# Kernel optimization log

Measured on AMD Instinct MI355X. Metric: run time of the kernel, lower is better.

The kernel has to match this reference:

```python
import jax, jax.numpy as jnp
import numpy as np

LN_EPS = 1e-5  # torch nn.LayerNorm default

def _layer_norm(x, g, b):
    mu = x.mean(axis=-1, keepdims=True)
    var = x.var(axis=-1, keepdims=True)
    return (x - mu) / jnp.sqrt(var + LN_EPS) * g + b

def setup_inputs() -> dict:
    key = jax.random.key(0)
    ks = jax.random.split(key, 8)
    B, T, L = 1, 4, 384
    c_z, c_t, H, C = 128, 64, 4, 16
    s = 0.02
    t = jax.random.normal(ks[0], (B, T, L, L, c_t), dtype=jnp.float32)
    z = jax.random.normal(ks[1], (B, L, L, c_z), dtype=jnp.float32)
    template_mask = jax.random.randint(ks[2], (B, T, L), 0, 2).astype(jnp.float32)
    Wq = jax.random.normal(ks[3], (c_z, H * C), dtype=jnp.float32) * s
    Wk = jax.random.normal(ks[4], (c_t, H * C), dtype=jnp.float32) * s
    Wv = jax.random.normal(ks[5], (c_t, H * C), dtype=jnp.float32) * s
    Wo = jax.random.normal(ks[6], (H * C, c_z), dtype=jnp.float32) * s
    bo = jnp.zeros((c_z,), dtype=jnp.float32)
    z_ln_g = jnp.ones((c_z,), dtype=jnp.float32)
    z_ln_b = jnp.zeros((c_z,), dtype=jnp.float32)
    t_ln_g = jnp.ones((c_t,), dtype=jnp.float32)
    t_ln_b = jnp.zeros((c_t,), dtype=jnp.float32)
    return dict(t=t, z=z, template_mask=template_mask,
                z_ln_g=z_ln_g, z_ln_b=z_ln_b, t_ln_g=t_ln_g, t_ln_b=t_ln_b,
                Wq=Wq, Wk=Wk, Wv=Wv, Wo=Wo, bo=bo)

def reference(t, z, template_mask, z_ln_g, z_ln_b, t_ln_g, t_ln_b, Wq, Wk, Wv, Wo, bo):
    B, T, L = t.shape[0], t.shape[1], t.shape[2]
    H, C = 4, 16
    z_norm = _layer_norm(z, z_ln_g, z_ln_b)          # [B,L,L,c_z]
    t_norm = _layer_norm(t, t_ln_g, t_ln_b)          # [B,T,L,L,c_t]
    q = (z_norm @ Wq).reshape(B, L, L, H, C)          # [B,L,L,H,C]
    k = (t_norm @ Wk).reshape(B, T, L, L, H, C)       # [B,T,L,L,H,C]
    v = (t_norm @ Wv).reshape(B, T, L, L, H, C)
    logits = jnp.einsum('bijhc,btijhc->btijh', q, k) / jnp.sqrt(jnp.float32(C))
    # pair_mask[b,t,i,j] = m[b,t,i]*m[b,t,j]
    pair_mask = template_mask[:, :, :, None] * template_mask[:, :, None, :]  # [B,T,L,L]
    logits = jnp.where(pair_mask[..., None] == 0, jnp.float32(-1e9), logits)
    attn = jax.nn.softmax(logits, axis=1)             # softmax over template dim T
    attn = attn * pair_mask[..., None]
    attn = attn / jnp.clip(attn.sum(axis=1, keepdims=True), 1e-8, None)
    out = jnp.einsum('btijh,btijhc->bijhc', attn, v).reshape(B, L, L, H * C)
    return out @ Wo + bo
```

## Files before the change

### kernel.cpp

```cpp
#include <hip/hip_runtime.h>

typedef unsigned int u32;
typedef unsigned short u16;
typedef __attribute__((ext_vector_type(8))) short short8;
typedef __attribute__((ext_vector_type(4))) float f4;

#define MFMA(a, b, c) __builtin_amdgcn_mfma_f32_16x16x32_bf16((a), (b), (c), 0, 0, 0)
#define LL 384
#define NPAIR 147456

__device__ __forceinline__ u16 f2bf(float f) {
    u32 u = __float_as_uint(f);
    u = (u + 0x7fffu + ((u >> 16) & 1u)) >> 16;
    return (u16)u;
}
__device__ __forceinline__ u32 pack2(float a, float b) {
    u32 ua = __float_as_uint(a); ua = (ua + 0x7fffu + ((ua >> 16) & 1u)) >> 16;
    u32 ub = __float_as_uint(b); ub = (ub + 0x7fffu + ((ub >> 16) & 1u)) >> 16;
    return ua | (ub << 16);
}
__device__ __forceinline__ short8 ld8(const u16* p) { return *reinterpret_cast<const short8*>(p); }

template <int CTRL>
__device__ __forceinline__ float dpp_add(float v) {
    int t = __builtin_amdgcn_update_dpp(0, __float_as_int(v), CTRL, 0xf, 0xf, true);
    return v + __int_as_float(t);
}
__device__ __forceinline__ float red16(float v) {
    v = dpp_add<0xB1>(v);
    v = dpp_add<0x4E>(v);
    v = dpp_add<0x124>(v);
    v = dpp_add<0x128>(v);
    return v;
}


__global__ void prep_w(const float* __restrict__ Wq, const float* __restrict__ Wk,
                       const float* __restrict__ Wv, const float* __restrict__ Wo,
                       const float* __restrict__ zg, const float* __restrict__ tg,
                       float* __restrict__ ws) {
    int idx = blockIdx.x * blockDim.x + threadIdx.x;
    u16* wsu = (u16*)ws;
    if (idx < 8192) {
        int kb = idx >> 9, rem = idx & 511, n = rem >> 3, j = rem & 7, k = kb * 8 + j;
        wsu[idx] = f2bf(Wq[k * 64 + n] * zg[k]);
    } else if (idx < 12288) {
        int e = idx - 8192;
        int kb = e >> 9, rem = e & 511, n = rem >> 3, j = rem & 7, k = kb * 8 + j;
        wsu[idx] = f2bf(Wk[k * 64 + n] * tg[k]);
    } else if (idx < 16384) {
        int e = idx - 12288;
        int kb = e >> 9, rem = e & 511, n = rem >> 3, j = rem & 7, k = kb * 8 + j;
        wsu[idx] = f2bf(Wv[k * 64 + n] * tg[k]);
    } else if (idx < 24576) {
        int e = idx - 16384;
        int kb = e >> 10, rem = e & 1023, n = rem >> 3, j = rem & 7, k = kb * 8 + j;
        wsu[idx] = f2bf(Wo[k * 128 + n]);
    }
}

__global__ void prep_aux(const float* __restrict__ Wq, const float* __restrict__ Wk,
                         const float* __restrict__ Wv, const float* __restrict__ zg,
                         const float* __restrict__ zb, const float* __restrict__ tg,
                         const float* __restrict__ tb, const float* __restrict__ bo,
                         float* __restrict__ ws) {
    int idx = blockIdx.x * blockDim.x + threadIdx.x;
    if (idx < 384) {
        int g = idx >> 6, hc = idx & 63;
        float acc = 0.f;
        if (g == 0)      { for (int d = 0; d < 128; ++d) acc += zg[d] * Wq[d*64+hc]; ws[12288+hc] = acc; }
        else if (g == 1) { for (int d = 0; d < 128; ++d) acc += zb[d] * Wq[d*64+hc]; ws[12352+hc] = acc; }
        else if (g == 2) { for (int d = 0; d < 64;  ++d) acc += tg[d] * Wk[d*64+hc]; ws[12416+hc] = acc; }
        else if (g == 3) { for (int d = 0; d < 64;  ++d) acc += tb[d] * Wk[d*64+hc]; ws[12480+hc] = acc; }
        else if (g == 4) { for (int d = 0; d < 64;  ++d) acc += tg[d] * Wv[d*64+hc]; ws[12544+hc] = acc; }
        else             { for (int d = 0; d < 64;  ++d) acc += tb[d] * Wv[d*64+hc]; ws[12608+hc] = acc; }
    } else if (idx < 512) {
        ws[12672 + idx - 384] = bo[idx - 384];
    }
}

__global__ __launch_bounds__(256, 5) void tpa_main(
    const float* __restrict__ tmpl,
    const float* __restrict__ z,
    const float* __restrict__ mask,
    const float* __restrict__ ws,
    float* __restrict__ out)
{
    __shared__ __align__(16) u16 sT[4 * 32 * 72];
    __shared__ __align__(16) u16 sZ[32 * 136];
    __shared__ float sZr[32], sZrm[32];
    __shared__ float sTr[4 * 32], sTrm[4 * 32];
    __shared__ float sAux[384];
    __shared__ float sBo[128];
    __shared__ float sPm[4 * 32];

    const int tid = threadIdx.x;
    const int p0 = blockIdx.x * 32;
    const u16* wsu = (const u16*)ws;

    if (tid < 128) {
        sAux[tid]       = ws[12288 + tid];
        sAux[128 + tid] = ws[12416 + tid];
        sAux[256 + tid] = ws[12544 + tid];
        sBo[tid]        = ws[12672 + tid];
        int tt = tid >> 5, rr = tid & 31;
        int p = p0 + rr, i = p / LL, j = p - i * LL;
        sPm[tt * 32 + rr] = mask[tt * LL + i] * mask[tt * LL + j];
    }
    {
        int pp = tid >> 3, part = tid & 7;
        const float4* zg4 = (const float4*)(z + (size_t)(p0 + pp) * 128) + part * 4;
        float4 a0 = zg4[0], a1 = zg4[1], a2 = zg4[2], a3 = zg4[3];
        float s = a0.x+a0.y+a0.z+a0.w + a1.x+a1.y+a1.z+a1.w
                + a2.x+a2.y+a2.z+a2.w + a3.x+a3.y+a3.z+a3.w;
        float ss = a0.x*a0.x+a0.y*a0.y+a0.z*a0.z+a0.w*a0.w
                 + a1.x*a1.x+a1.y*a1.y+a1.z*a1.z+a1.w*a1.w
                 + a2.x*a2.x+a2.y*a2.y+a2.z*a2.z+a2.w*a2.w
                 + a3.x*a3.x+a3.y*a3.y+a3.z*a3.z+a3.w*a3.w;
        s += __shfl_xor(s, 1); ss += __shfl_xor(ss, 1);
        s += __shfl_xor(s, 2); ss += __shfl_xor(ss, 2);
        s += __shfl_xor(s, 4); ss += __shfl_xor(ss, 4);
        if (part == 0) {
            float mu = s * (1.f / 128.f);
            float var = fmaf(-mu, mu, ss * (1.f / 128.f));
            float r = rsqrtf(var + 1e-5f);
            sZr[pp] = r; sZrm[pp] = r * mu;
        }
        uint4 w0, w1;
        w0.x = pack2(a0.x, a0.y); w0.y = pack2(a0.z, a0.w);
        w0.z = pack2(a1.x, a1.y); w0.w = pack2(a1.z, a1.w);
        w1.x = pack2(a2.x, a2.y); w1.y = pack2(a2.z, a2.w);
        w1.z = pack2(a3.x, a3.y); w1.w = pack2(a3.z, a3.w);
        uint4* d = (uint4*)(sZ + pp * 136 + part * 16);
        d[0] = w0; d[1] = w1;
    }
    {
        int tt = tid >> 6, pp = (tid >> 1) & 31, part = tid & 1;
        const float4* tg4 = (const float4*)(tmpl + ((size_t)tt * NPAIR + p0 + pp) * 64) + part * 8;
        float s = 0.f, ss = 0.f;
        uint4 wbuf[4];
        #pragma unroll
        for (int c = 0; c < 4; ++c) {
            float4 b0 = tg4[c * 2], b1 = tg4[c * 2 + 1];
            s  += b0.x+b0.y+b0.z+b0.w + b1.x+b1.y+b1.z+b1.w;
            ss += b0.x*b0.x+b0.y*b0.y+b0.z*b0.z+b0.w*b0.w
                + b1.x*b1.x+b1.y*b1.y+b1.z*b1.z+b1.w*b1.w;
            wbuf[c].x = pack2(b0.x, b0.y); wbuf[c].y = pack2(b0.z, b0.w);
            wbuf[c].z = pack2(b1.x, b1.y); wbuf[c].w = pack2(b1.z, b1.w);
        }
        s += __shfl_xor(s, 1); ss += __shfl_xor(ss, 1);
        if (part == 0) {
            float mu = s * (1.f / 64.f);
            float var = fmaf(-mu, mu, ss * (1.f / 64.f));
            float r = rsqrtf(var + 1e-5f);
            sTr[tt * 32 + pp] = r; sTrm[tt * 32 + pp] = r * mu;
        }
        uint4* d = (uint4*)(sT + tt * 2304 + pp * 72 + part * 32);
        d[0] = wbuf[0]; d[1] = wbuf[1]; d[2] = wbuf[2]; d[3] = wbuf[3];
    }
    __syncthreads();

    const int wave = tid >> 6, lane = tid & 63, g = lane >> 4, l15 = lane & 15;
    const int rt = wave & 1, nh = wave >> 1;
    const int rowA = rt * 16 + l15;
    const int col0 = (2 * nh) * 16 + l15, col1 = (2 * nh + 1) * 16 + l15;
    int rowC[4];
    #pragma unroll
    for (int r = 0; r < 4; ++r) rowC[r] = rt * 16 + g * 4 + r;

    f4 aq0 = {0.f,0.f,0.f,0.f}, aq1 = {0.f,0.f,0.f,0.f};
    #pragma unroll
    for (int ks = 0; ks < 4; ++ks) {
        short8 A = ld8(sZ + rowA * 136 + ks * 32 + g * 8);
        const u16* wb = wsu + (ks * 4 + g) * 512;
        aq0 = MFMA(A, ld8(wb + col0 * 8), aq0);
        aq1 = MFMA(A, ld8(wb + col1 * 8), aq1);
    }
    float qv[2][4];
    {
        float GQ0 = sAux[col0], BQ0 = sAux[64 + col0];
        float GQ1 = sAux[col1], BQ1 = sAux[64 + col1];
        #pragma unroll
        for (int r = 0; r < 4; ++r) {
            float zr = sZr[rowC[r]], zm = sZrm[rowC[r]];
            qv[0][r] = 0.25f * fmaf(zr, aq0[r], fmaf(-zm, GQ0, BQ0));
            qv[1][r] = 0.25f * fmaf(zr, aq1[r], fmaf(-zm, GQ1, BQ1));
        }
    }

    float lg[4][2][4];
    {
        const u16* wk = wsu + 8192;
        short8 Bk00 = ld8(wk + g * 512 + col0 * 8);
        short8 Bk01 = ld8(wk + g * 512 + col1 * 8);
        short8 Bk10 = ld8(wk + (4 + g) * 512 + col0 * 8);
        short8 Bk11 = ld8(wk + (4 + g) * 512 + col1 * 8);
        float GK0 = sAux[128 + col0], BK0 = sAux[192 + col0];
        float GK1 = sAux[128 + col1], BK1 = sAux[192 + col1];
        #pragma unroll
        for (int tt = 0; tt < 4; ++tt) {
            const u16* At = sT + tt * 2304 + rowA * 72;
            short8 A0 = ld8(At + g * 8);
            short8 A1 = ld8(At + 32 + g * 8);
            f4 k0 = {0.f,0.f,0.f,0.f}, k1 = {0.f,0.f,0.f,0.f};
            k0 = MFMA(A0, Bk00, k0); k1 = MFMA(A0, Bk01, k1);
            k0 = MFMA(A1, Bk10, k0); k1 = MFMA(A1, Bk11, k1);
            #pragma unroll
            for (int r = 0; r < 4; ++r) {
                float tr = sTr[tt * 32 + rowC[r]], tm = sTrm[tt * 32 + rowC[r]];
                float kc0 = fmaf(tr, k0[r], fmaf(-tm, GK0, BK0));
                float kc1 = fmaf(tr, k1[r], fmaf(-tm, GK1, BK1));
                lg[tt][0][r] = red16(qv[0][r] * kc0);
                lg[tt][1][r] = red16(qv[1][r] * kc1);
            }
        }
    }

    float ap[4][2][4], cb[2][4], cg[2][4];
    #pragma unroll
    for (int r = 0; r < 4; ++r) {
        float trA[4], tmA[4], pmA[4];
        #pragma unroll
        for (int tt = 0; tt < 4; ++tt) {
            trA[tt] = sTr[tt * 32 + rowC[r]];
            tmA[tt] = sTrm[tt * 32 + rowC[r]];
            pmA[tt] = sPm[tt * 32 + rowC[r]];
        }
        #pragma unroll
        for (int nn = 0; nn < 2; ++nn) {
            float l0 = lg[0][nn][r], l1 = lg[1][nn][r], l2 = lg[2][nn][r], l3 = lg[3][nn][r];
            float mx = fmaxf(fmaxf(l0, l1), fmaxf(l2, l3));
            float e0 = __expf(l0 - mx) * pmA[0];
            float e1 = __expf(l1 - mx) * pmA[1];
            float e2 = __expf(l2 - mx) * pmA[2];
            float e3 = __expf(l3 - mx) * pmA[3];
            float s = (e0 + e1) + (e2 + e3);
            float rr = __builtin_amdgcn_rcpf(fmaxf(s, 1e-20f));
            float a0 = e0 * rr, a1 = e1 * rr, a2 = e2 * rr, a3 = e3 * rr;
            cb[nn][r] = s * rr;
            cg[nn][r] = a0 * tmA[0] + a1 * tmA[1] + a2 * tmA[2] + a3 * tmA[3];
            ap[0][nn][r] = a0 * trA[0]; ap[1][nn][r] = a1 * trA[1];
            ap[2][nn][r] = a2 * trA[2]; ap[3][nn][r] = a3 * trA[3];
        }
    }

    float o0[4] = {0.f,0.f,0.f,0.f}, o1[4] = {0.f,0.f,0.f,0.f};
    {
        const u16* wv = wsu + 12288;
        short8 Bv00 = ld8(wv + g * 512 + col0 * 8);
        short8 Bv01 = ld8(wv + g * 512 + col1 * 8);
        short8 Bv10 = ld8(wv + (4 + g) * 512 + col0 * 8);
        short8 Bv11 = ld8(wv + (4 + g) * 512 + col1 * 8);
        #pragma unroll
        for (int tt = 0; tt < 4; ++tt) {
            const u16* At = sT + tt * 2304 + rowA * 72;
            short8 A0 = ld8(At + g * 8);
            short8 A1 = ld8(At + 32 + g * 8);
            f4 v0 = {0.f,0.f,0.f,0.f}, v1 = {0.f,0.f,0.f,0.f};
            v0 = MFMA(A0, Bv00, v0); v1 = MFMA(A0, Bv01, v1);
            v0 = MFMA(A1, Bv10, v0); v1 = MFMA(A1, Bv11, v1);
            #pragma unroll
            for (int r = 0; r < 4; ++r) {
                o0[r] = fmaf(ap[tt][0][r], v0[r], o0[r]);
                o1[r] = fmaf(ap[tt][1][r], v1[r], o1[r]);
            }
        }
        float GV0 = sAux[256 + col0], BV0 = sAux[320 + col0];
        float GV1 = sAux[256 + col1], BV1 = sAux[320 + col1];
        #pragma unroll
        for (int r = 0; r < 4; ++r) {
            o0[r] = fmaf(cb[0][r], BV0, fmaf(-cg[0][r], GV0, o0[r]));
            o1[r] = fmaf(cb[1][r], BV1, fmaf(-cg[1][r], GV1, o1[r]));
        }
    }
    __syncthreads();
    {
        #pragma unroll
        for (int r = 0; r < 4; ++r) {
            sZ[rowC[r] * 72 + col0] = f2bf(o0[r]);
            sZ[rowC[r] * 72 + col1] = f2bf(o1[r]);
        }
    }
    __syncthreads();

    {
        const u16* wo = wsu + 16384;
        const int nb = (wave >> 1) * 4;
        f4 c0 = {0.f,0.f,0.f,0.f}, c1 = {0.f,0.f,0.f,0.f};
        f4 c2 = {0.f,0.f,0.f,0.f}, c3 = {0.f,0.f,0.f,0.f};
        #pragma unroll
        for (int ks = 0; ks < 2; ++ks) {
            short8 A = ld8(sZ + rowA * 72 + ks * 32 + g * 8);
            const u16* wb = wo + (ks * 4 + g) * 1024;
            c0 = MFMA(A, ld8(wb + ((nb + 0) * 16 + l15) * 8), c0);
            c1 = MFMA(A, ld8(wb + ((nb + 1) * 16 + l15) * 8), c1);
            c2 = MFMA(A, ld8(wb + ((nb + 2) * 16 + l15) * 8), c2);
            c3 = MFMA(A, ld8(wb + ((nb + 3) * 16 + l15) * 8), c3);
        }
        #pragma unroll
        for (int r = 0; r < 4; ++r) {
            int row = p0 + rowC[r];
            float* op = out + (size_t)row * 128;
            op[(nb + 0) * 16 + l15] = c0[r] + sBo[(nb + 0) * 16 + l15];
            op[(nb + 1) * 16 + l15] = c1[r] + sBo[(nb + 1) * 16 + l15];
            op[(nb + 2) * 16 + l15] = c2[r] + sBo[(nb + 2) * 16 + l15];
            op[(nb + 3) * 16 + l15] = c3[r] + sBo[(nb + 3) * 16 + l15];
        }
    }
}

extern "C" void kernel_launch(void* const* d_in, const int* in_sizes, int n_in,
                              void* d_out, int out_size, void* d_ws, size_t ws_size,
                              hipStream_t stream) {
    const float* t   = (const float*)d_in[0];
    const float* z   = (const float*)d_in[1];
    const float* msk = (const float*)d_in[2];
    const float* zg  = (const float*)d_in[3];
    const float* zb  = (const float*)d_in[4];
    const float* tg  = (const float*)d_in[5];
    const float* tb  = (const float*)d_in[6];
    const float* Wq  = (const float*)d_in[7];
    const float* Wk  = (const float*)d_in[8];
    const float* Wv  = (const float*)d_in[9];
    const float* Wo  = (const float*)d_in[10];
    const float* bo  = (const float*)d_in[11];
    float* ws = (float*)d_ws;

    prep_w<<<96, 256, 0, stream>>>(Wq, Wk, Wv, Wo, zg, tg, ws);
    prep_aux<<<2, 256, 0, stream>>>(Wq, Wk, Wv, zg, zb, tg, tb, bo, ws);
    tpa_main<<<4608, 256, 0, stream>>>(t, z, msk, ws, (float*)d_out);
}
```

Measured before the change: 366.0 us.

## Load template and z straight into MFMA fragments, dropping LDS staging

Drops the LDS staging of z and the template tiles. Each lane now loads its own rows from global memory, packs them to bf16 in registers as MFMA A-fragments, and computes the LayerNorm statistics with cross-lane shuffles. The template is read from global a second time for the V projection, which relies on cache hits. The softmax max-subtraction is removed, and the output tile goes through a small XOR-swizzled LDS buffer with one fewer barrier. Occupancy hint drops from 5 to 4 blocks. This trades LDS traffic and barriers for extra global reads and register pressure, and skipping the max-subtraction risks overflow if logits are large.

After: 479.9 us. 1.31x slower.

```diff
diff --git a/kernel.cpp b/kernel.cpp
--- a/kernel.cpp
+++ b/kernel.cpp
@@ -20,6 +20,12 @@
     return ua | (ub << 16);
 }
 __device__ __forceinline__ short8 ld8(const u16* p) { return *reinterpret_cast<const short8*>(p); }
+__device__ __forceinline__ short8 to8(u32 a, u32 b, u32 c, u32 d) {
+    union { u32 u[4]; short8 s; } x; x.u[0] = a; x.u[1] = b; x.u[2] = c; x.u[3] = d; return x.s;
+}
+__device__ __forceinline__ short8 frag8(float4 c0, float4 c1) {
+    return to8(pack2(c0.x, c0.y), pack2(c0.z, c0.w), pack2(c1.x, c1.y), pack2(c1.z, c1.w));
+}
 
 template <int CTRL>
 __device__ __forceinline__ float dpp_add(float v) {
@@ -32,6 +38,10 @@
     v = dpp_add<0x124>(v);
     v = dpp_add<0x128>(v);
     return v;
+}
+
+__device__ __forceinline__ int swz128(int row, int bcol) {
+    return row * 128 + (bcol ^ ((row & 7) << 4));
 }
 
 
@@ -79,135 +89,100 @@
     }
 }
 
-__global__ __launch_bounds__(256, 5) void tpa_main(
+__global__ __launch_bounds__(256, 4) void tpa_main(
     const float* __restrict__ tmpl,
     const float* __restrict__ z,
     const float* __restrict__ mask,
     const float* __restrict__ ws,
     float* __restrict__ out)
 {
-    __shared__ __align__(16) u16 sT[4 * 32 * 72];
-    __shared__ __align__(16) u16 sZ[32 * 136];
-    __shared__ float sZr[32], sZrm[32];
-    __shared__ float sTr[4 * 32], sTrm[4 * 32];
-    __shared__ float sAux[384];
-    __shared__ float sBo[128];
-    __shared__ float sPm[4 * 32];
+    __shared__ __align__(16) u16 sO[32 * 64];
 
     const int tid = threadIdx.x;
     const int p0 = blockIdx.x * 32;
     const u16* wsu = (const u16*)ws;
-
-    if (tid < 128) {
-        sAux[tid]       = ws[12288 + tid];
-        sAux[128 + tid] = ws[12416 + tid];
-        sAux[256 + tid] = ws[12544 + tid];
-        sBo[tid]        = ws[12672 + tid];
-        int tt = tid >> 5, rr = tid & 31;
-        int p = p0 + rr, i = p / LL, j = p - i * LL;
-        sPm[tt * 32 + rr] = mask[tt * LL + i] * mask[tt * LL + j];
-    }
-    {
-        int pp = tid >> 3, part = tid & 7;
-        const float4* zg4 = (const float4*)(z + (size_t)(p0 + pp) * 128) + part * 4;
-        float4 a0 = zg4[0], a1 = zg4[1], a2 = zg4[2], a3 = zg4[3];
-        float s = a0.x+a0.y+a0.z+a0.w + a1.x+a1.y+a1.z+a1.w
-                + a2.x+a2.y+a2.z+a2.w + a3.x+a3.y+a3.z+a3.w;
-        float ss = a0.x*a0.x+a0.y*a0.y+a0.z*a0.z+a0.w*a0.w
-                 + a1.x*a1.x+a1.y*a1.y+a1.z*a1.z+a1.w*a1.w
-                 + a2.x*a2.x+a2.y*a2.y+a2.z*a2.z+a2.w*a2.w
-                 + a3.x*a3.x+a3.y*a3.y+a3.z*a3.z+a3.w*a3.w;
-        s += __shfl_xor(s, 1); ss += __shfl_xor(ss, 1);
-        s += __shfl_xor(s, 2); ss += __shfl_xor(ss, 2);
-        s += __shfl_xor(s, 4); ss += __shfl_xor(ss, 4);
-        if (part == 0) {
-            float mu = s * (1.f / 128.f);
-            float var = fmaf(-mu, mu, ss * (1.f / 128.f));
-            float r = rsqrtf(var + 1e-5f);
-            sZr[pp] = r; sZrm[pp] = r * mu;
-        }
-        uint4 w0, w1;
-        w0.x = pack2(a0.x, a0.y); w0.y = pack2(a0.z, a0.w);
-        w0.z = pack2(a1.x, a1.y); w0.w = pack2(a1.z, a1.w);
-        w1.x = pack2(a2.x, a2.y); w1.y = pack2(a2.z, a2.w);
-        w1.z = pack2(a3.x, a3.y); w1.w = pack2(a3.z, a3.w);
-        uint4* d = (uint4*)(sZ + pp * 136 + part * 16);
-        d[0] = w0; d[1] = w1;
-    }
-    {
-        int tt = tid >> 6, pp = (tid >> 1) & 31, part = tid & 1;
-        const float4* tg4 = (const float4*)(tmpl + ((size_t)tt * NPAIR + p0 + pp) * 64) + part * 8;
-        float s = 0.f, ss = 0.f;
-        uint4 wbuf[4];
-        #pragma unroll
-        for (int c = 0; c < 4; ++c) {
-            float4 b0 = tg4[c * 2], b1 = tg4[c * 2 + 1];
-            s  += b0.x+b0.y+b0.z+b0.w + b1.x+b1.y+b1.z+b1.w;
-            ss += b0.x*b0.x+b0.y*b0.y+b0.z*b0.z+b0.w*b0.w
-                + b1.x*b1.x+b1.y*b1.y+b1.z*b1.z+b1.w*b1.w;
-            wbuf[c].x = pack2(b0.x, b0.y); wbuf[c].y = pack2(b0.z, b0.w);
-            wbuf[c].z = pack2(b1.x, b1.y); wbuf[c].w = pack2(b1.z, b1.w);
-        }
-        s += __shfl_xor(s, 1); ss += __shfl_xor(ss, 1);
-        if (part == 0) {
-            float mu = s * (1.f / 64.f);
-            float var = fmaf(-mu, mu, ss * (1.f / 64.f));
-            float r = rsqrtf(var + 1e-5f);
-            sTr[tt * 32 + pp] = r; sTrm[tt * 32 + pp] = r * mu;
-        }
-        uint4* d = (uint4*)(sT + tt * 2304 + pp * 72 + part * 32);
-        d[0] = wbuf[0]; d[1] = wbuf[1]; d[2] = wbuf[2]; d[3] = wbuf[3];
-    }
-    __syncthreads();
+    const float* wsf = ws;
+    char* sOb = (char*)sO;
 
     const int wave = tid >> 6, lane = tid & 63, g = lane >> 4, l15 = lane & 15;
     const int rt = wave & 1, nh = wave >> 1;
     const int rowA = rt * 16 + l15;
+    const int gp = p0 + rowA;
     const int col0 = (2 * nh) * 16 + l15, col1 = (2 * nh + 1) * 16 + l15;
     int rowC[4];
     #pragma unroll
     for (int r = 0; r < 4; ++r) rowC[r] = rt * 16 + g * 4 + r;
 
+    float GK0 = wsf[12416 + col0], GK1 = wsf[12416 + col1];
+    float BK0 = wsf[12480 + col0], BK1 = wsf[12480 + col1];
+
     f4 aq0 = {0.f,0.f,0.f,0.f}, aq1 = {0.f,0.f,0.f,0.f};
-    #pragma unroll
-    for (int ks = 0; ks < 4; ++ks) {
-        short8 A = ld8(sZ + rowA * 136 + ks * 32 + g * 8);
-        const u16* wb = wsu + (ks * 4 + g) * 512;
-        aq0 = MFMA(A, ld8(wb + col0 * 8), aq0);
-        aq1 = MFMA(A, ld8(wb + col1 * 8), aq1);
-    }
+    float s = 0.f, ss = 0.f;
+    {
+        const float4* zp = (const float4*)(z + (size_t)gp * 128);
+        #pragma unroll
+        for (int ks = 0; ks < 4; ++ks) {
+            float4 c0 = zp[ks * 8 + g * 2], c1 = zp[ks * 8 + g * 2 + 1];
+            s  += c0.x+c0.y+c0.z+c0.w + c1.x+c1.y+c1.z+c1.w;
+            ss += c0.x*c0.x+c0.y*c0.y+c0.z*c0.z+c0.w*c0.w
+                + c1.x*c1.x+c1.y*c1.y+c1.z*c1.z+c1.w*c1.w;
+            short8 A = frag8(c0, c1);
+            const u16* wb = wsu + (ks * 4 + g) * 512;
+            aq0 = MFMA(A, ld8(wb + col0 * 8), aq0);
+            aq1 = MFMA(A, ld8(wb + col1 * 8), aq1);
+        }
+    }
+    s += __shfl_xor(s, 16); ss += __shfl_xor(ss, 16);
+    s += __shfl_xor(s, 32); ss += __shfl_xor(ss, 32);
     float qv[2][4];
     {
-        float GQ0 = sAux[col0], BQ0 = sAux[64 + col0];
-        float GQ1 = sAux[col1], BQ1 = sAux[64 + col1];
+        float zmu = s * (1.f / 128.f);
+        float zvar = fmaf(-zmu, zmu, ss * (1.f / 128.f));
+        float zr = rsqrtf(zvar + 1e-5f), zrm = zr * zmu;
+        float GQ0 = wsf[12288 + col0], GQ1 = wsf[12288 + col1];
+        float BQ0 = wsf[12352 + col0], BQ1 = wsf[12352 + col1];
         #pragma unroll
         for (int r = 0; r < 4; ++r) {
-            float zr = sZr[rowC[r]], zm = sZrm[rowC[r]];
-            qv[0][r] = 0.25f * fmaf(zr, aq0[r], fmaf(-zm, GQ0, BQ0));
-            qv[1][r] = 0.25f * fmaf(zr, aq1[r], fmaf(-zm, GQ1, BQ1));
+            int src = g * 4 + r;
+            float zrS = __shfl(zr, src), zmS = __shfl(zrm, src);
+            qv[0][r] = 0.25f * fmaf(zrS, aq0[r], fmaf(-zmS, GQ0, BQ0));
+            qv[1][r] = 0.25f * fmaf(zrS, aq1[r], fmaf(-zmS, GQ1, BQ1));
         }
     }
 
     float lg[4][2][4];
-    {
-        const u16* wk = wsu + 8192;
+    float trS[4][4], tmS[4][4];
+    const u16* wk = wsu + 8192;
+    {
         short8 Bk00 = ld8(wk + g * 512 + col0 * 8);
         short8 Bk01 = ld8(wk + g * 512 + col1 * 8);
         short8 Bk10 = ld8(wk + (4 + g) * 512 + col0 * 8);
         short8 Bk11 = ld8(wk + (4 + g) * 512 + col1 * 8);
-        float GK0 = sAux[128 + col0], BK0 = sAux[192 + col0];
-        float GK1 = sAux[128 + col1], BK1 = sAux[192 + col1];
         #pragma unroll
         for (int tt = 0; tt < 4; ++tt) {
-            const u16* At = sT + tt * 2304 + rowA * 72;
-            short8 A0 = ld8(At + g * 8);
-            short8 A1 = ld8(At + 32 + g * 8);
+            const float4* tp = (const float4*)(tmpl + ((size_t)tt * NPAIR + gp) * 64);
+            float4 c0 = tp[g * 2], c1 = tp[g * 2 + 1];
+            float4 c2 = tp[8 + g * 2], c3 = tp[8 + g * 2 + 1];
+            float s2  = c0.x+c0.y+c0.z+c0.w + c1.x+c1.y+c1.z+c1.w
+                      + c2.x+c2.y+c2.z+c2.w + c3.x+c3.y+c3.z+c3.w;
+            float ss2 = c0.x*c0.x+c0.y*c0.y+c0.z*c0.z+c0.w*c0.w
+                      + c1.x*c1.x+c1.y*c1.y+c1.z*c1.z+c1.w*c1.w
+                      + c2.x*c2.x+c2.y*c2.y+c2.z*c2.z+c2.w*c2.w
+                      + c3.x*c3.x+c3.y*c3.y+c3.z*c3.z+c3.w*c3.w;
+            s2 += __shfl_xor(s2, 16); ss2 += __shfl_xor(ss2, 16);
+            s2 += __shfl_xor(s2, 32); ss2 += __shfl_xor(ss2, 32);
+            float mu = s2 * (1.f / 64.f);
+            float var = fmaf(-mu, mu, ss2 * (1.f / 64.f));
+            float rr = rsqrtf(var + 1e-5f), rm = rr * mu;
+            short8 A0 = frag8(c0, c1), A1 = frag8(c2, c3);
             f4 k0 = {0.f,0.f,0.f,0.f}, k1 = {0.f,0.f,0.f,0.f};
             k0 = MFMA(A0, Bk00, k0); k1 = MFMA(A0, Bk01, k1);
             k0 = MFMA(A1, Bk10, k0); k1 = MFMA(A1, Bk11, k1);
             #pragma unroll
             for (int r = 0; r < 4; ++r) {
-                float tr = sTr[tt * 32 + rowC[r]], tm = sTrm[tt * 32 + rowC[r]];
+                int src = g * 4 + r;
+                float tr = __shfl(rr, src), tm = __shfl(rm, src);
+                trS[tt][r] = tr; tmS[tt][r] = tm;
                 float kc0 = fmaf(tr, k0[r], fmaf(-tm, GK0, BK0));
                 float kc1 = fmaf(tr, k1[r], fmaf(-tm, GK1, BK1));
                 lg[tt][0][r] = red16(qv[0][r] * kc0);
@@ -216,31 +191,28 @@
         }
     }
 
-    float ap[4][2][4], cb[2][4], cg[2][4];
+    float cb[2][4], cg[2][4];
     #pragma unroll
     for (int r = 0; r < 4; ++r) {
-        float trA[4], tmA[4], pmA[4];
-        #pragma unroll
-        for (int tt = 0; tt < 4; ++tt) {
-            trA[tt] = sTr[tt * 32 + rowC[r]];
-            tmA[tt] = sTrm[tt * 32 + rowC[r]];
-            pmA[tt] = sPm[tt * 32 + rowC[r]];
-        }
+        int p = p0 + rowC[r], i = p / LL, j = p - i * LL;
+        float pmA[4];
+        #pragma unroll
+        for (int tt = 0; tt < 4; ++tt) pmA[tt] = mask[tt * LL + i] * mask[tt * LL + j];
         #pragma unroll
         for (int nn = 0; nn < 2; ++nn) {
-            float l0 = lg[0][nn][r], l1 = lg[1][nn][r], l2 = lg[2][nn][r], l3 = lg[3][nn][r];
-            float mx = fmaxf(fmaxf(l0, l1), fmaxf(l2, l3));
-            float e0 = __expf(l0 - mx) * pmA[0];
-            float e1 = __expf(l1 - mx) * pmA[1];
-            float e2 = __expf(l2 - mx) * pmA[2];
-            float e3 = __expf(l3 - mx) * pmA[3];
-            float s = (e0 + e1) + (e2 + e3);
-            float rr = __builtin_amdgcn_rcpf(fmaxf(s, 1e-20f));
-            float a0 = e0 * rr, a1 = e1 * rr, a2 = e2 * rr, a3 = e3 * rr;
-            cb[nn][r] = s * rr;
-            cg[nn][r] = a0 * tmA[0] + a1 * tmA[1] + a2 * tmA[2] + a3 * tmA[3];
-            ap[0][nn][r] = a0 * trA[0]; ap[1][nn][r] = a1 * trA[1];
-            ap[2][nn][r] = a2 * trA[2]; ap[3][nn][r] = a3 * trA[3];
+            float e0 = __expf(lg[0][nn][r]) * pmA[0];
+            float e1 = __expf(lg[1][nn][r]) * pmA[1];
+            float e2 = __expf(lg[2][nn][r]) * pmA[2];
+            float e3 = __expf(lg[3][nn][r]) * pmA[3];
+            float sm = (e0 + e1) + (e2 + e3);
+            float rr2 = __builtin_amdgcn_rcpf(fmaxf(sm, 1e-20f));
+            float a0 = e0 * rr2, a1 = e1 * rr2, a2 = e2 * rr2, a3 = e3 * rr2;
+            cb[nn][r] = sm * rr2;
+            cg[nn][r] = a0 * tmS[0][r] + a1 * tmS[1][r] + a2 * tmS[2][r] + a3 * tmS[3][r];
+            lg[0][nn][r] = a0 * trS[0][r];
+            lg[1][nn][r] = a1 * trS[1][r];
+            lg[2][nn][r] = a2 * trS[2][r];
+            lg[3][nn][r] = a3 * trS[3][r];
         }
     }
 
@@ -253,44 +225,43 @@
         short8 Bv11 = ld8(wv + (4 + g) * 512 + col1 * 8);
         #pragma unroll
         for (int tt = 0; tt < 4; ++tt) {
-            const u16* At = sT + tt * 2304 + rowA * 72;
-            short8 A0 = ld8(At + g * 8);
-            short8 A1 = ld8(At + 32 + g * 8);
+            const float4* tp = (const float4*)(tmpl + ((size_t)tt * NPAIR + gp) * 64);
+            short8 A0 = frag8(tp[g * 2], tp[g * 2 + 1]);
+            short8 A1 = frag8(tp[8 + g * 2], tp[8 + g * 2 + 1]);
             f4 v0 = {0.f,0.f,0.f,0.f}, v1 = {0.f,0.f,0.f,0.f};
             v0 = MFMA(A0, Bv00, v0); v1 = MFMA(A0, Bv01, v1);
             v0 = MFMA(A1, Bv10, v0); v1 = MFMA(A1, Bv11, v1);
             #pragma unroll
             for (int r = 0; r < 4; ++r) {
-                o0[r] = fmaf(ap[tt][0][r], v0[r], o0[r]);
-                o1[r] = fmaf(ap[tt][1][r], v1[r], o1[r]);
+                o0[r] = fmaf(lg[tt][0][r], v0[r], o0[r]);
+                o1[r] = fmaf(lg[tt][1][r], v1[r], o1[r]);
             }
         }
-        float GV0 = sAux[256 + col0], BV0 = sAux[320 + col0];
-        float GV1 = sAux[256 + col1], BV1 = sAux[320 + col1];
+        float GV0 = wsf[12544 + col0], GV1 = wsf[12544 + col1];
+        float BV0 = wsf[12608 + col0], BV1 = wsf[12608 + col1];
         #pragma unroll
         for (int r = 0; r < 4; ++r) {
             o0[r] = fmaf(cb[0][r], BV0, fmaf(-cg[0][r], GV0, o0[r]));
             o1[r] = fmaf(cb[1][r], BV1, fmaf(-cg[1][r], GV1, o1[r]));
         }
     }
+
+    #pragma unroll
+    for (int r = 0; r < 4; ++r) {
+        u32 p = pack2(o0[r], o1[r]);
+        *(u16*)(sOb + swz128(rowC[r], col0 * 2)) = (u16)p;
+        *(u16*)(sOb + swz128(rowC[r], col1 * 2)) = (u16)(p >> 16);
+    }
     __syncthreads();
-    {
-        #pragma unroll
-        for (int r = 0; r < 4; ++r) {
-            sZ[rowC[r] * 72 + col0] = f2bf(o0[r]);
-            sZ[rowC[r] * 72 + col1] = f2bf(o1[r]);
-        }
-    }
-    __syncthreads();
 
     {
         const u16* wo = wsu + 16384;
-        const int nb = (wave >> 1) * 4;
+        const int nb = nh * 4;
         f4 c0 = {0.f,0.f,0.f,0.f}, c1 = {0.f,0.f,0.f,0.f};
         f4 c2 = {0.f,0.f,0.f,0.f}, c3 = {0.f,0.f,0.f,0.f};
         #pragma unroll
         for (int ks = 0; ks < 2; ++ks) {
-            short8 A = ld8(sZ + rowA * 72 + ks * 32 + g * 8);
+            short8 A = ld8((const u16*)(sOb + swz128(rowA, (ks * 4 + g) * 16)));
             const u16* wb = wo + (ks * 4 + g) * 1024;
             c0 = MFMA(A, ld8(wb + ((nb + 0) * 16 + l15) * 8), c0);
             c1 = MFMA(A, ld8(wb + ((nb + 1) * 16 + l15) * 8), c1);
@@ -301,10 +272,10 @@
         for (int r = 0; r < 4; ++r) {
             int row = p0 + rowC[r];
             float* op = out + (size_t)row * 128;
-            op[(nb + 0) * 16 + l15] = c0[r] + sBo[(nb + 0) * 16 + l15];
-            op[(nb + 1) * 16 + l15] = c1[r] + sBo[(nb + 1) * 16 + l15];
-            op[(nb + 2) * 16 + l15] = c2[r] + sBo[(nb + 2) * 16 + l15];
-            op[(nb + 3) * 16 + l15] = c3[r] + sBo[(nb + 3) * 16 + l15];
+            op[(nb + 0) * 16 + l15] = c0[r] + wsf[12672 + (nb + 0) * 16 + l15];
+            op[(nb + 1) * 16 + l15] = c1[r] + wsf[12672 + (nb + 1) * 16 + l15];
+            op[(nb + 2) * 16 + l15] = c2[r] + wsf[12672 + (nb + 2) * 16 + l15];
+            op[(nb + 3) * 16 + l15] = c3[r] + wsf[12672 + (nb + 3) * 16 + l15];
         }
     }
 }
```
